# Optimization experiments

Hardware: AMD Instinct MI355X
Metric: run time of the kernel (lower is better)

Reference implementation:

```python
import jax, jax.numpy as jnp
import numpy as np

# LinearMoELayer(input_size=2048, output_size=2048, num_experts=8, num_selects=2,
#                bias=True, gate_network='mlp', gate_use_balance=True,
#                gate_add_noise=True, gate_use_softmax=True)
# Eval-mode forward semantics (deterministic: noise branch only active in training).
B, S, D, O, E, K = 4, 2048, 2048, 2048, 8, 2
BAL_W = 1e-2   # balance_loss_weight
EPS = 1e-10    # cv_squared eps


def setup_inputs() -> dict:
    key = jax.random.key(0)
    ks = jax.random.split(key, 5)
    x = jax.random.normal(ks[0], (B, S, D), dtype=jnp.float32)
    # gate 'mlp': Linear(D,E,bias=False) -> tanh -> Linear(E,E,bias=False)
    gate_w1 = jax.random.normal(ks[1], (E, D), dtype=jnp.float32) * (1.0 / np.sqrt(D))
    gate_w2 = jax.random.normal(ks[2], (E, E), dtype=jnp.float32) * (1.0 / np.sqrt(E))
    # LinearExperts: per-expert weight [E, O, D] and bias [E, O] (F.linear convention)
    expert_w = jax.random.normal(ks[3], (E, O, D), dtype=jnp.float32) * (1.0 / np.sqrt(D))
    expert_b = jax.random.normal(ks[4], (E, O), dtype=jnp.float32) * 0.01
    return {"x": x, "gate_w1": gate_w1, "gate_w2": gate_w2,
            "expert_w": expert_w, "expert_b": expert_b}


def _cv_squared(v):
    # torch: v.var() / (v.mean()**2 + eps); torch.var is unbiased (ddof=1)
    m = jnp.mean(v)
    var = jnp.sum((v - m) ** 2) / (v.shape[0] - 1)
    return var / (m * m + EPS)


def reference(x, gate_w1, gate_w2, expert_w, expert_b):
    xt = x.reshape(-1, D)                                  # [T, D]
    T = xt.shape[0]
    # --- TopKBalancedNoisyGate (eval path) ---
    logits = jnp.tanh(xt @ gate_w1.T) @ gate_w2.T          # [T, E]
    top_logits, top_idx = jax.lax.top_k(logits, K)         # [T, K]
    scores = jax.nn.softmax(top_logits.astype(jnp.float32), axis=-1)  # [T, K]
    # scatter top-k scores into dense [T, E] gate matrix
    dense = jnp.zeros((T, E), dtype=scores.dtype)
    dense = dense.at[jnp.arange(T)[:, None], top_idx].set(scores)
    importance = dense.sum(axis=0)                         # [E]
    load = (dense > 0).sum(axis=0).astype(jnp.float32)     # [E] token counts
    gate_loss = BAL_W * (_cv_squared(importance) + _cv_squared(load))
    # --- UniversalCalculator: per-expert linear + score-weighted combine ---
    # math-equivalent to sort/dispatch/grouped-linear/index_add combine
    h = jnp.einsum('td,eod->teo', xt, expert_w) + expert_b[None, :, :]  # [T, E, O]
    y = jnp.einsum('te,teo->to', dense, h)                 # [T, O]
    return y.reshape(B, S, O), gate_loss
```

## Files before the change

kernel.cpp:

```cpp
#include <hip/hip_runtime.h>
#include <hip/hip_bf16.h>

#define TT 8192
#define DD 2048
#define OO 2048
#define EE 8

typedef __attribute__((ext_vector_type(4))) float f32x4;
typedef __attribute__((ext_vector_type(8))) short s16x8;
typedef __attribute__((ext_vector_type(4))) short s16x4;

__device__ __forceinline__ short f2bf(float f) {
    union { float f; unsigned u; } v; v.f = f;
    unsigned r = (v.u + 0x7FFFu + ((v.u >> 16) & 1u)) >> 16;
    return (short)(unsigned short)r;
}
__device__ __forceinline__ float bf2f(short s) {
    union { unsigned u; float f; } v; v.u = ((unsigned)(unsigned short)s) << 16;
    return v.f;
}

__global__ __launch_bounds__(256) void cvt_bf16_kernel(const float* __restrict__ in,
                                                       short* __restrict__ out, long n8) {
    long i = (long)blockIdx.x * blockDim.x + threadIdx.x;
    long stride = (long)gridDim.x * blockDim.x;
    for (; i < n8; i += stride) {
        f32x4 a = ((const f32x4*)in)[i * 2];
        f32x4 b = ((const f32x4*)in)[i * 2 + 1];
        s16x8 r;
        r[0] = f2bf(a[0]); r[1] = f2bf(a[1]); r[2] = f2bf(a[2]); r[3] = f2bf(a[3]);
        r[4] = f2bf(b[0]); r[5] = f2bf(b[1]); r[6] = f2bf(b[2]); r[7] = f2bf(b[3]);
        ((s16x8*)out)[i] = r;
    }
}

__global__ __launch_bounds__(256) void gate_kernel(
    const float* __restrict__ x, const float* __restrict__ w1, const float* __restrict__ w2,
    int* __restrict__ tk_idx, float* __restrict__ tk_score)
{
    const int lane = threadIdx.x & 63;
    const int wid = threadIdx.x >> 6;
    const int t = blockIdx.x * 4 + wid;
    const float* xt = x + (long)t * DD;

    float acc[8] = {0.f,0.f,0.f,0.f,0.f,0.f,0.f,0.f};
#pragma unroll
    for (int i = 0; i < DD / 256; ++i) {
        f32x4 xv = *(const f32x4*)&xt[i * 256 + lane * 4];
#pragma unroll
        for (int e2 = 0; e2 < 8; ++e2) {
            f32x4 wv = *(const f32x4*)&w1[e2 * DD + i * 256 + lane * 4];
            acc[e2] += xv[0]*wv[0] + xv[1]*wv[1] + xv[2]*wv[2] + xv[3]*wv[3];
        }
    }
#pragma unroll
    for (int e2 = 0; e2 < 8; ++e2) {
#pragma unroll
        for (int off = 32; off > 0; off >>= 1)
            acc[e2] += __shfl_xor(acc[e2], off, 64);
    }

    float th[8], lg[8];
#pragma unroll
    for (int e2 = 0; e2 < 8; ++e2) th[e2] = tanhf(acc[e2]);
#pragma unroll
    for (int eo = 0; eo < 8; ++eo) {
        float s = 0.f;
#pragma unroll
        for (int e2 = 0; e2 < 8; ++e2) s += th[e2] * w2[eo * 8 + e2];
        lg[eo] = s;
    }
    int e0 = 0;
#pragma unroll
    for (int q = 1; q < 8; ++q) if (lg[q] > lg[e0]) e0 = q;
    int e1 = (e0 == 0) ? 1 : 0;
#pragma unroll
    for (int q = 0; q < 8; ++q) if (q != e0 && lg[q] > lg[e1]) e1 = q;

    float d = expf(lg[e1] - lg[e0]);
    float s0 = 1.f / (1.f + d);
    float s1 = d / (1.f + d);

    if (lane == 0) {
        tk_idx[t * 2] = e0; tk_idx[t * 2 + 1] = e1;
        tk_score[t * 2] = s0; tk_score[t * 2 + 1] = s1;
    }
}

__global__ __launch_bounds__(256) void build_lists(
    const int* __restrict__ tk_idx, const float* __restrict__ tk_score,
    int* __restrict__ tok_list, float* __restrict__ score_list, int* __restrict__ cnt,
    float* __restrict__ imp)
{
    const int e = blockIdx.x;
    const int lane = threadIdx.x & 63;
    const int wid = threadIdx.x >> 6;
    __shared__ int wsum[4];
    __shared__ float wsumF[4];
    int base = 0;
    float ssum = 0.f;
    for (int t0 = 0; t0 < TT; t0 += 256) {
        int t = t0 + threadIdx.x;
        int i0 = tk_idx[t * 2], i1 = tk_idx[t * 2 + 1];
        bool has = (i0 == e) || (i1 == e);
        int slot = (i0 == e) ? 0 : 1;
        float sc = (i0 == e) ? tk_score[t * 2] : tk_score[t * 2 + 1];
        unsigned long long m = __ballot(has);
        int prefix = __popcll(m & ((1ull << lane) - 1ull));
        if (lane == 0) wsum[wid] = __popcll(m);
        __syncthreads();
        int woff = 0;
#pragma unroll
        for (int w = 0; w < 4; ++w) woff += (w < wid) ? wsum[w] : 0;
        int total = wsum[0] + wsum[1] + wsum[2] + wsum[3];
        if (has) {
            int p = base + woff + prefix;
            tok_list[e * TT + p] = t * 2 + slot;
            score_list[e * TT + p] = sc;
            ssum += sc;
        }
        base += total;
        __syncthreads();
    }
#pragma unroll
    for (int off = 32; off > 0; off >>= 1)
        ssum += __shfl_xor(ssum, off, 64);
    if (lane == 0) wsumF[wid] = ssum;
    __syncthreads();
    if (threadIdx.x == 0) {
        cnt[e] = base;
        imp[e] = wsumF[0] + wsumF[1] + wsumF[2] + wsumF[3];
    }
}

__global__ __launch_bounds__(64) void loss_finalize(const float* __restrict__ imp,
                                                    const int* __restrict__ cnt,
                                                    float* __restrict__ loss_out)
{
    if (threadIdx.x == 0) {
        float im[8], ld[8];
        float mi = 0.f, ml = 0.f;
#pragma unroll
        for (int q = 0; q < 8; ++q) {
            im[q] = imp[q]; ld[q] = (float)cnt[q];
            mi += im[q]; ml += ld[q];
        }
        mi *= 0.125f; ml *= 0.125f;
        float vi = 0.f, vl = 0.f;
#pragma unroll
        for (int q = 0; q < 8; ++q) {
            float a = im[q] - mi; vi += a * a;
            float b = ld[q] - ml; vl += b * b;
        }
        vi /= 7.f; vl /= 7.f;
        loss_out[0] = 0.01f * (vi / (mi * mi + 1e-10f) + vl / (ml * ml + 1e-10f));
    }
}

__global__ __launch_bounds__(256) void combine_kernel(float* __restrict__ y,
                                                      const short* __restrict__ part1) {
    long i = (long)blockIdx.x * blockDim.x + threadIdx.x;
    long stride = (long)gridDim.x * blockDim.x;
    const long n4 = (long)TT * OO / 4;
    for (; i < n4; i += stride) {
        f32x4 v = ((const f32x4*)y)[i];
        s16x4 p = ((const s16x4*)part1)[i];
        v[0] += bf2f(p[0]); v[1] += bf2f(p[1]);
        v[2] += bf2f(p[2]); v[3] += bf2f(p[3]);
        ((f32x4*)y)[i] = v;
    }
}

#define GLD16(gsrc, ldst) \
    __builtin_amdgcn_global_load_lds((const __attribute__((address_space(1))) unsigned int*)(gsrc), \
                                     (__attribute__((address_space(3))) unsigned int*)(ldst), 16, 0, 0)

#define BAR() __builtin_amdgcn_s_barrier()

__global__ __launch_bounds__(512, 2) void moe_gemm(
    const short* __restrict__ xbf, const short* __restrict__ wbf,
    const float* __restrict__ eb,
    const int* __restrict__ tok_list, const float* __restrict__ score_list,
    const int* __restrict__ cnt, float* __restrict__ y, short* __restrict__ part1)
{
    const int e = blockIdx.z;
    const int n_e = cnt[e];
    const int xb = blockIdx.x, yb = blockIdx.y;
    const int cb = ((xb >> 2) << 2) + (yb & 3);
    const int rb = (xb & 3) + ((yb >> 2) << 2);
    const int row0 = rb * 256;
    if (row0 >= n_e) return;
    const int col0 = cb * 256;

    __shared__ alignas(16) short lds[2 * 32768];
    __shared__ int   stok[256];
    __shared__ float ssc[256];

    const int tid = threadIdx.x;
    const int lane = tid & 63;
    const int wid = tid >> 6;
    const int wr = wid >> 2, wc = wid & 3;
    const int fr = lane & 15, fq = lane >> 4;
    const char* ldsb = (const char*)lds;

    if (tid < 256) {
        int slot = row0 + tid;
        if (slot >= n_e) slot = n_e - 1;
        stok[tid] = tok_list[e * TT + slot];
        ssc[tid]  = score_list[e * TT + slot];
    }
    __syncthreads();

    const int r_ = tid >> 3;
    const int csw = ((tid & 7) ^ (r_ & 7)) * 8;
    const short* aS[4];
#pragma unroll
    for (int g = 0; g < 4; ++g)
        aS[g] = xbf + (long)(stok[g * 64 + r_] >> 1) * DD + csw;
    const short* bS[4];
#pragma unroll
    for (int g = 0; g < 4; ++g)
        bS[g] = wbf + (long)e * OO * DD + (long)(col0 + g * 64 + r_) * DD + csw;

#define STAGE_A(g, kt) GLD16(aS[g] + (kt) * 64, (char*)lds + ((kt) & 1) * 65536 + ((g) * 512 + tid) * 16)
#define STAGE_B(g, kt) GLD16(bS[g] + (kt) * 64, (char*)lds + ((kt) & 1) * 65536 + 32768 + ((g) * 512 + tid) * 16)

    const int aBase = (wr * 128 + fr) * 128;
    const int bBase = 32768 + (wc * 64 + fr) * 128;
    const int sw0 = (fq ^ (fr & 7)) * 16;
    const int sw1 = ((fq + 4) ^ (fr & 7)) * 16;

    f32x4 acc[8][4];
#pragma unroll
    for (int m = 0; m < 8; ++m)
#pragma unroll
        for (int n = 0; n < 4; ++n) acc[m][n] = f32x4{0.f, 0.f, 0.f, 0.f};

    STAGE_A(0, 0); STAGE_A(1, 0); STAGE_A(2, 0); STAGE_A(3, 0);
    STAGE_B(0, 0); STAGE_B(1, 0); STAGE_B(2, 0); STAGE_B(3, 0);
    STAGE_A(0, 1); STAGE_A(1, 1);
    asm volatile("s_waitcnt vmcnt(2)");
    BAR();

#pragma unroll 1
    for (int j = 0; j < DD / 64; ++j) {
        const int fb = (j & 1) * 65536;
        const bool st1 = (j + 1) < DD / 64;
        const bool st2 = (j + 2) < DD / 64;

        s16x8 a0[4][2], a1[4][2], bb[4][2];

#pragma unroll
        for (int mm = 0; mm < 4; ++mm) {
            a0[mm][0] = *(const s16x8*)(ldsb + fb + aBase + mm * 2048 + sw0);
            a0[mm][1] = *(const s16x8*)(ldsb + fb + aBase + mm * 2048 + sw1);
        }
#pragma unroll
        for (int n = 0; n < 4; ++n) {
            bb[n][0] = *(const s16x8*)(ldsb + fb + bBase + n * 2048 + sw0);
            bb[n][1] = *(const s16x8*)(ldsb + fb + bBase + n * 2048 + sw1);
        }
        if (st1) {
            STAGE_A(2, j + 1); STAGE_A(3, j + 1);
            STAGE_B(0, j + 1); STAGE_B(1, j + 1);
            STAGE_B(2, j + 1); STAGE_B(3, j + 1);
        }
        __builtin_amdgcn_s_setprio(1);
#pragma unroll
        for (int mm = 0; mm < 4; ++mm)
#pragma unroll
            for (int n = 0; n < 4; ++n) {
                acc[mm][n] = __builtin_amdgcn_mfma_f32_16x16x32_bf16(a0[mm][0], bb[n][0], acc[mm][n], 0, 0, 0);
                acc[mm][n] = __builtin_amdgcn_mfma_f32_16x16x32_bf16(a0[mm][1], bb[n][1], acc[mm][n], 0, 0, 0);
            }
        __builtin_amdgcn_s_setprio(0);
#pragma unroll
        for (int mm = 0; mm < 4; ++mm) {
            a1[mm][0] = *(const s16x8*)(ldsb + fb + aBase + 8192 + mm * 2048 + sw0);
            a1[mm][1] = *(const s16x8*)(ldsb + fb + aBase + 8192 + mm * 2048 + sw1);
        }
        __builtin_amdgcn_s_setprio(1);
#pragma unroll
        for (int mm = 0; mm < 4; ++mm)
#pragma unroll
            for (int n = 0; n < 4; ++n) {
                acc[4 + mm][n] = __builtin_amdgcn_mfma_f32_16x16x32_bf16(a1[mm][0], bb[n][0], acc[4 + mm][n], 0, 0, 0);
                acc[4 + mm][n] = __builtin_amdgcn_mfma_f32_16x16x32_bf16(a1[mm][1], bb[n][1], acc[4 + mm][n], 0, 0, 0);
            }
        __builtin_amdgcn_s_setprio(0);

        BAR();
        if (st2) { STAGE_A(0, j + 2); STAGE_A(1, j + 2); }
        if (st2) { asm volatile("s_waitcnt vmcnt(2)"); }
        else     { asm volatile("s_waitcnt vmcnt(0)"); }
        BAR();
    }

    float bval[4];
#pragma unroll
    for (int n = 0; n < 4; ++n)
        bval[n] = eb[e * OO + col0 + wc * 64 + n * 16 + fr];

#pragma unroll
    for (int m = 0; m < 8; ++m) {
#pragma unroll
        for (int jj = 0; jj < 4; ++jj) {
            int tslot = wr * 128 + m * 16 + fq * 4 + jj;
            if (row0 + tslot < n_e) {
                int packed = stok[tslot];
                int t = packed >> 1;
                float s = ssc[tslot];
                if ((packed & 1) == 0) {
#pragma unroll
                    for (int n = 0; n < 4; ++n) {
                        int o = col0 + wc * 64 + n * 16 + fr;
                        y[(long)t * OO + o] = s * (acc[m][n][jj] + bval[n]);
                    }
                } else {
#pragma unroll
                    for (int n = 0; n < 4; ++n) {
                        int o = col0 + wc * 64 + n * 16 + fr;
                        part1[(long)t * OO + o] = f2bf(s * (acc[m][n][jj] + bval[n]));
                    }
                }
            }
        }
    }
#undef STAGE_A
#undef STAGE_B
}

extern "C" void kernel_launch(void* const* d_in, const int* in_sizes, int n_in,
                              void* d_out, int out_size, void* d_ws, size_t ws_size,
                              hipStream_t stream) {
    const float* x  = (const float*)d_in[0];
    const float* w1 = (const float*)d_in[1];
    const float* w2 = (const float*)d_in[2];
    const float* ew = (const float*)d_in[3];
    const float* eb = (const float*)d_in[4];
    float* y = (float*)d_out;

    char* ws = (char*)d_ws;
    short* xbf = (short*)ws;            ws += (size_t)TT * DD * 2;
    short* wbf = (short*)ws;            ws += (size_t)EE * OO * DD * 2;
    short* part1 = (short*)ws;          ws += (size_t)TT * OO * 2;
    int*   tok_list = (int*)ws;         ws += (size_t)EE * TT * 4;
    float* score_list = (float*)ws;     ws += (size_t)EE * TT * 4;
    int*   tk_idx = (int*)ws;           ws += (size_t)TT * 2 * 4;
    float* tk_score = (float*)ws;       ws += (size_t)TT * 2 * 4;
    int*   cnt = (int*)ws;              ws += 64;
    float* imp = (float*)ws;            ws += 64;

    cvt_bf16_kernel<<<8192, 256, 0, stream>>>(ew, wbf, (long)EE * OO * DD / 8);
    cvt_bf16_kernel<<<4096, 256, 0, stream>>>(x,  xbf, (long)TT * DD / 8);
    gate_kernel<<<TT / 4, 256, 0, stream>>>(x, w1, w2, tk_idx, tk_score);
    build_lists<<<EE, 256, 0, stream>>>(tk_idx, tk_score, tok_list, score_list, cnt, imp);
    loss_finalize<<<1, 64, 0, stream>>>(imp, cnt, y + (size_t)TT * OO);
    moe_gemm<<<dim3(8, 32, EE), 512, 0, stream>>>(
        xbf, wbf, eb, tok_list, score_list, cnt, y, part1);
    combine_kernel<<<2048, 256, 0, stream>>>(y, part1);
}
```

Measured before the change: 310.9 us.

## Merge conversion kernels, store both expert partials as bf16, reorder LDS reads

Fuses the weight and activation fp32-to-bf16 conversions into one launch. The GEMM epilogue now writes both top-k partial outputs as bf16 into separate buffers instead of one fp32 write to y, and combine reads two bf16 buffers and writes y. This removes the fp32 read of y in combine and halves the GEMM's first-slot store traffic. In exchange it adds a workspace buffer and rounds the first partial to bf16, losing precision. Global-to-LDS staging for the next tile is also issued before the current LDS fragment reads.

```diff
diff --git a/kernel.cpp b/kernel.cpp
--- a/kernel.cpp
+++ b/kernel.cpp
@@ -20,17 +20,23 @@
     return v.f;
 }
 
-__global__ __launch_bounds__(256) void cvt_bf16_kernel(const float* __restrict__ in,
-                                                       short* __restrict__ out, long n8) {
+__global__ __launch_bounds__(256) void cvt_both_kernel(
+    const float* __restrict__ ew, short* __restrict__ wbf, long n8w,
+    const float* __restrict__ x, short* __restrict__ xbf, long n8x)
+{
     long i = (long)blockIdx.x * blockDim.x + threadIdx.x;
     long stride = (long)gridDim.x * blockDim.x;
-    for (; i < n8; i += stride) {
-        f32x4 a = ((const f32x4*)in)[i * 2];
-        f32x4 b = ((const f32x4*)in)[i * 2 + 1];
+    long total = n8w + n8x;
+    for (; i < total; i += stride) {
+        const float* in; short* out; long k;
+        if (i < n8w) { in = ew; out = wbf; k = i; }
+        else         { in = x;  out = xbf; k = i - n8w; }
+        f32x4 a = ((const f32x4*)in)[k * 2];
+        f32x4 b = ((const f32x4*)in)[k * 2 + 1];
         s16x8 r;
         r[0] = f2bf(a[0]); r[1] = f2bf(a[1]); r[2] = f2bf(a[2]); r[3] = f2bf(a[3]);
         r[4] = f2bf(b[0]); r[5] = f2bf(b[1]); r[6] = f2bf(b[2]); r[7] = f2bf(b[3]);
-        ((s16x8*)out)[i] = r;
+        ((s16x8*)out)[k] = r;
     }
 }
 
@@ -158,15 +164,19 @@
 }
 
 __global__ __launch_bounds__(256) void combine_kernel(float* __restrict__ y,
+                                                      const short* __restrict__ part0,
                                                       const short* __restrict__ part1) {
     long i = (long)blockIdx.x * blockDim.x + threadIdx.x;
     long stride = (long)gridDim.x * blockDim.x;
     const long n4 = (long)TT * OO / 4;
     for (; i < n4; i += stride) {
-        f32x4 v = ((const f32x4*)y)[i];
-        s16x4 p = ((const s16x4*)part1)[i];
-        v[0] += bf2f(p[0]); v[1] += bf2f(p[1]);
-        v[2] += bf2f(p[2]); v[3] += bf2f(p[3]);
+        s16x4 p0 = ((const s16x4*)part0)[i];
+        s16x4 p1 = ((const s16x4*)part1)[i];
+        f32x4 v;
+        v[0] = bf2f(p0[0]) + bf2f(p1[0]);
+        v[1] = bf2f(p0[1]) + bf2f(p1[1]);
+        v[2] = bf2f(p0[2]) + bf2f(p1[2]);
+        v[3] = bf2f(p0[3]) + bf2f(p1[3]);
         ((f32x4*)y)[i] = v;
     }
 }
@@ -181,7 +191,7 @@
     const short* __restrict__ xbf, const short* __restrict__ wbf,
     const float* __restrict__ eb,
     const int* __restrict__ tok_list, const float* __restrict__ score_list,
-    const int* __restrict__ cnt, float* __restrict__ y, short* __restrict__ part1)
+    const int* __restrict__ cnt, short* __restrict__ part0, short* __restrict__ part1)
 {
     const int e = blockIdx.z;
     const int n_e = cnt[e];
@@ -250,20 +260,20 @@
 
         s16x8 a0[4][2], a1[4][2], bb[4][2];
 
-#pragma unroll
-        for (int mm = 0; mm < 4; ++mm) {
-            a0[mm][0] = *(const s16x8*)(ldsb + fb + aBase + mm * 2048 + sw0);
-            a0[mm][1] = *(const s16x8*)(ldsb + fb + aBase + mm * 2048 + sw1);
-        }
-#pragma unroll
-        for (int n = 0; n < 4; ++n) {
-            bb[n][0] = *(const s16x8*)(ldsb + fb + bBase + n * 2048 + sw0);
-            bb[n][1] = *(const s16x8*)(ldsb + fb + bBase + n * 2048 + sw1);
-        }
         if (st1) {
             STAGE_A(2, j + 1); STAGE_A(3, j + 1);
             STAGE_B(0, j + 1); STAGE_B(1, j + 1);
             STAGE_B(2, j + 1); STAGE_B(3, j + 1);
+        }
+#pragma unroll
+        for (int mm = 0; mm < 4; ++mm) {
+            a0[mm][0] = *(const s16x8*)(ldsb + fb + aBase + mm * 2048 + sw0);
+            a0[mm][1] = *(const s16x8*)(ldsb + fb + aBase + mm * 2048 + sw1);
+        }
+#pragma unroll
+        for (int n = 0; n < 4; ++n) {
+            bb[n][0] = *(const s16x8*)(ldsb + fb + bBase + n * 2048 + sw0);
+            bb[n][1] = *(const s16x8*)(ldsb + fb + bBase + n * 2048 + sw1);
         }
         __builtin_amdgcn_s_setprio(1);
 #pragma unroll
@@ -310,18 +320,11 @@
                 int packed = stok[tslot];
                 int t = packed >> 1;
                 float s = ssc[tslot];
-                if ((packed & 1) == 0) {
-#pragma unroll
-                    for (int n = 0; n < 4; ++n) {
-                        int o = col0 + wc * 64 + n * 16 + fr;
-                        y[(long)t * OO + o] = s * (acc[m][n][jj] + bval[n]);
-                    }
-                } else {
-#pragma unroll
-                    for (int n = 0; n < 4; ++n) {
-                        int o = col0 + wc * 64 + n * 16 + fr;
-                        part1[(long)t * OO + o] = f2bf(s * (acc[m][n][jj] + bval[n]));
-                    }
+                short* dst = ((packed & 1) == 0) ? part0 : part1;
+#pragma unroll
+                for (int n = 0; n < 4; ++n) {
+                    int o = col0 + wc * 64 + n * 16 + fr;
+                    dst[(long)t * OO + o] = f2bf(s * (acc[m][n][jj] + bval[n]));
                 }
             }
         }
@@ -343,6 +346,7 @@
     char* ws = (char*)d_ws;
     short* xbf = (short*)ws;            ws += (size_t)TT * DD * 2;
     short* wbf = (short*)ws;            ws += (size_t)EE * OO * DD * 2;
+    short* part0 = (short*)ws;          ws += (size_t)TT * OO * 2;
     short* part1 = (short*)ws;          ws += (size_t)TT * OO * 2;
     int*   tok_list = (int*)ws;         ws += (size_t)EE * TT * 4;
     float* score_list = (float*)ws;     ws += (size_t)EE * TT * 4;
@@ -351,12 +355,12 @@
     int*   cnt = (int*)ws;              ws += 64;
     float* imp = (float*)ws;            ws += 64;
 
-    cvt_bf16_kernel<<<8192, 256, 0, stream>>>(ew, wbf, (long)EE * OO * DD / 8);
-    cvt_bf16_kernel<<<4096, 256, 0, stream>>>(x,  xbf, (long)TT * DD / 8);
+    cvt_both_kernel<<<8192, 256, 0, stream>>>(ew, wbf, (long)EE * OO * DD / 8,
+                                              x, xbf, (long)TT * DD / 8);
     gate_kernel<<<TT / 4, 256, 0, stream>>>(x, w1, w2, tk_idx, tk_score);
     build_lists<<<EE, 256, 0, stream>>>(tk_idx, tk_score, tok_list, score_list, cnt, imp);
     loss_finalize<<<1, 64, 0, stream>>>(imp, cnt, y + (size_t)TT * OO);
     moe_gemm<<<dim3(8, 32, EE), 512, 0, stream>>>(
-        xbf, wbf, eb, tok_list, score_list, cnt, y, part1);
-    combine_kernel<<<2048, 256, 0, stream>>>(y, part1);
-}
+        xbf, wbf, eb, tok_list, score_list, cnt, part0, part1);
+    combine_kernel<<<2048, 256, 0, stream>>>(y, part0, part1);
+}
```

Result: slower. 331.5 us (+6.6%).
